# Kernel tuning notes

Measured on AMD Instinct MI355X. Metric: run time of the kernel, lower is better.

## Reference

```python
import jax, jax.numpy as jnp
from jax import lax
import numpy as np

POOLED_H = 7
POOLED_W = 7
SPATIAL_SCALE = 0.0625


def setup_inputs() -> dict:
    key = jax.random.key(0)
    kf, kx1, ky1, kw, kh = jax.random.split(key, 5)
    B, H, W, C = 1, 64, 64, 512
    N = 512
    img_h, img_w = H / SPATIAL_SCALE, W / SPATIAL_SCALE
    feat = jax.random.normal(kf, (B, H, W, C), dtype=jnp.float32)
    # rois: (batch_idx, x1, y1, x2, y2) in image coordinates, boxes inside image
    x1 = jax.random.uniform(kx1, (N,), minval=0.0, maxval=img_w * 0.8)
    y1 = jax.random.uniform(ky1, (N,), minval=0.0, maxval=img_h * 0.8)
    bw = jax.random.uniform(kw, (N,), minval=16.0, maxval=img_w * 0.5)
    bh = jax.random.uniform(kh, (N,), minval=16.0, maxval=img_h * 0.5)
    x2 = jnp.clip(x1 + bw, 0.0, img_w - 1.0)
    y2 = jnp.clip(y1 + bh, 0.0, img_h - 1.0)
    bidx = jnp.zeros((N,), dtype=jnp.float32)
    rois = jnp.stack([bidx, x1, y1, x2, y2], axis=1).astype(jnp.float32)
    return {"feat": feat, "rois": rois}


def _roi_pool(feat, rois, pooled_h, pooled_w, spatial_scale):
    B, H, W, C = feat.shape
    N = rois.shape[0]
    # max extent of a single bin (Caffe: hend-hstart <= bin_size + 2 <= H/pooled_h + 2)
    MBH = int(np.ceil(H / pooled_h)) + 2
    MBW = int(np.ceil(W / pooled_w)) + 2

    roi_batch = rois[:, 0].astype(jnp.int32)
    start_w = jnp.round(rois[:, 1] * spatial_scale).astype(jnp.int32)
    start_h = jnp.round(rois[:, 2] * spatial_scale).astype(jnp.int32)
    end_w = jnp.round(rois[:, 3] * spatial_scale).astype(jnp.int32)
    end_h = jnp.round(rois[:, 4] * spatial_scale).astype(jnp.int32)
    roi_h = jnp.maximum(end_h - start_h + 1, 1).astype(jnp.float32)
    roi_w = jnp.maximum(end_w - start_w + 1, 1).astype(jnp.float32)
    bin_h = roi_h / pooled_h  # [N] float
    bin_w = roi_w / pooled_w

    ar_h = jnp.arange(MBH)
    ar_w = jnp.arange(MBW)

    def pool_one_bin(bin_idx):
        ph = bin_idx // pooled_w
        pw = bin_idx % pooled_w

        def per_roi(b, sh, sw, bh_, bw_):
            hstart = jnp.clip(jnp.floor(ph * bh_).astype(jnp.int32) + sh, 0, H)
            hend = jnp.clip(jnp.ceil((ph + 1) * bh_).astype(jnp.int32) + sh, 0, H)
            wstart = jnp.clip(jnp.floor(pw * bw_).astype(jnp.int32) + sw, 0, W)
            wend = jnp.clip(jnp.ceil((pw + 1) * bw_).astype(jnp.int32) + sw, 0, W)
            empty = (hend <= hstart) | (wend <= wstart)
            # fixed-size window covering the bin; clamp start so slice stays in-bounds
            s_h = jnp.clip(hstart, 0, H - MBH)
            s_w = jnp.clip(wstart, 0, W - MBW)
            fmap = lax.dynamic_index_in_dim(feat, b, axis=0, keepdims=False)  # [H,W,C]
            patch = lax.dynamic_slice(fmap, (s_h, s_w, 0), (MBH, MBW, C))  # [MBH,MBW,C]
            rows = s_h + ar_h
            cols = s_w + ar_w
            valid = ((rows >= hstart) & (rows < hend))[:, None] & ((cols >= wstart) & (cols < wend))[None, :]
            neg = jnp.array(-jnp.inf, patch.dtype)
            mx = jnp.max(jnp.where(valid[:, :, None], patch, neg), axis=(0, 1))  # [C]
            return jnp.where(empty, jnp.zeros_like(mx), mx)

        return jax.vmap(per_roi)(roi_batch, start_h, start_w, bin_h, bin_w)  # [N,C]

    out = lax.map(pool_one_bin, jnp.arange(pooled_h * pooled_w))  # [PH*PW, N, C]
    out = out.transpose(1, 0, 2).reshape(N, pooled_h, pooled_w, C)
    return out


def reference(feat, rois):
    return _roi_pool(feat, rois, POOLED_H, POOLED_W, SPATIAL_SCALE)
```

## Files before the change

### kernel.cpp

```cpp
#include <hip/hip_runtime.h>
#include <cmath>

#define PH 7
#define PW 7
#define FH 64
#define FW 64
#define CC 512
#define SCALE 0.0625f

typedef float f32x4 __attribute__((ext_vector_type(4)));

static __device__ __forceinline__ f32x4 vmax4(f32x4 a, f32x4 b) {
    f32x4 r;
    r.x = fmaxf(a.x, b.x); r.y = fmaxf(a.y, b.y);
    r.z = fmaxf(a.z, b.z); r.w = fmaxf(a.w, b.w);
    return r;
}

__global__ __launch_bounds__(512) void sort_rois_kernel(
        const float* __restrict__ rois, int N, float4* __restrict__ geo) {
    __shared__ int base[64];
    __shared__ int cur[64];
    int t = threadIdx.x;
    if (t < 64) { base[t] = 0; cur[t] = 0; }
    __syncthreads();
    int b = -1, packed = 0;
    float bh = 0.f, bw = 0.f;
    if (t < N) {
        const float* r = rois + (size_t)t * 5;
        int bidx = (int)r[0];
        int sw = (int)rintf(r[1] * SCALE);
        int sh = (int)rintf(r[2] * SCALE);
        int ew = (int)rintf(r[3] * SCALE);
        int eh = (int)rintf(r[4] * SCALE);
        bh = fmaxf((float)(eh - sh + 1), 1.0f) * (1.0f / 7.0f);
        bw = fmaxf((float)(ew - sw + 1), 1.0f) * (1.0f / 7.0f);
        packed = t | (sh << 10) | (sw << 17) | (bidx << 24);
        b = min(max(sh, 0), FH - 1);
        atomicAdd(&base[b], 1);
    }
    __syncthreads();
    if (t == 0) {
        int acc = 0;
        for (int i = 0; i < 64; ++i) { int c = base[i]; base[i] = acc; acc += c; }
    }
    __syncthreads();
    if (t < N) {
        int pos = base[b] + atomicAdd(&cur[b], 1);
        float4 g;
        g.x = bh; g.y = bw; g.z = __int_as_float(packed); g.w = 0.f;
        geo[pos] = g;
    }
}

__global__ __launch_bounds__(256) void roi_pool_kernel(
        const float* __restrict__ feat,
        const float4* __restrict__ geo,
        float* __restrict__ out,
        int nBins) {
    int p = blockIdx.x;
    int nwg = gridDim.x;
    int q = nwg >> 3, rr = nwg & 7;
    int xcd = p & 7, o = p >> 3;
    int L = (xcd < rr ? xcd * (q + 1) : rr * (q + 1) + (xcd - rr) * q) + o;

    int tid = L * 256 + (int)threadIdx.x;
    int bin = tid >> 6;
    int lane = tid & 63;
    if (bin >= nBins) return;

    int s   = bin / (PH * PW);
    int rem = bin - s * (PH * PW);
    int ph  = rem / PW;
    int pw  = rem - ph * PW;

    float4 g = geo[s];
    float bh = g.x, bw = g.y;
    int packed = __float_as_int(g.z);
    int n    = packed & 1023;
    int sh   = (packed >> 10) & 127;
    int sw   = (packed >> 17) & 127;
    int bidx = (packed >> 24) & 255;

    int hstart = min(max((int)floorf((float)ph * bh) + sh, 0), FH);
    int hend   = min(max((int)ceilf((float)(ph + 1) * bh) + sh, 0), FH);
    int wstart = min(max((int)floorf((float)pw * bw) + sw, 0), FW);
    int wend   = min(max((int)ceilf((float)(pw + 1) * bw) + sw, 0), FW);

    int Wn = wend - wstart;
    int Hn = hend - hstart;
    bool empty = (Hn <= 0) || (Wn <= 0);

    f32x4 mxA = { -INFINITY, -INFINITY, -INFINITY, -INFINITY };
    f32x4 mxB = mxA;

    if (!empty) {
        unsigned cells = (unsigned)__builtin_amdgcn_readfirstlane(Hn * Wn);
        unsigned Wu    = (unsigned)__builtin_amdgcn_readfirstlane(Wn);
        unsigned wrap  = (unsigned)__builtin_amdgcn_readfirstlane((FW - Wn + 1) * CC);
        unsigned off0  = (unsigned)__builtin_amdgcn_readfirstlane(
            (bidx * FH * FW + hstart * FW + wstart) * CC);

        const float* fb = feat + off0;
        unsigned vo = (unsigned)lane * 4;

        unsigned soff = 0;
        unsigned cw = Wu;
        unsigned c = 0;
        unsigned quads = (cells + 3) >> 2;

#define ADV() do { if (--cw == 0) { soff += wrap; cw = Wu; } else soff += CC; } while (0)

        for (; quads; --quads) {
            unsigned o0 = soff;                          ADV();
            unsigned o1 = (c + 1 < cells) ? soff : 0u;   ADV();
            unsigned o2 = (c + 2 < cells) ? soff : 0u;   ADV();
            unsigned o3 = (c + 3 < cells) ? soff : 0u;   ADV();
            c += 4;
            const float* p0 = fb + o0;
            const float* p1 = fb + o1;
            const float* p2 = fb + o2;
            const float* p3 = fb + o3;
            f32x4 a0 = *(const f32x4*)(p0 + vo);  f32x4 b0 = *(const f32x4*)(p0 + vo + 256);
            f32x4 a1 = *(const f32x4*)(p1 + vo);  f32x4 b1 = *(const f32x4*)(p1 + vo + 256);
            f32x4 a2 = *(const f32x4*)(p2 + vo);  f32x4 b2 = *(const f32x4*)(p2 + vo + 256);
            f32x4 a3 = *(const f32x4*)(p3 + vo);  f32x4 b3 = *(const f32x4*)(p3 + vo + 256);
            a0 = vmax4(a0, a1); a2 = vmax4(a2, a3);
            b0 = vmax4(b0, b1); b2 = vmax4(b2, b3);
            mxA = vmax4(mxA, vmax4(a0, a2));
            mxB = vmax4(mxB, vmax4(b0, b2));
        }
#undef ADV
    } else {
        mxA = (f32x4){0.f, 0.f, 0.f, 0.f};
        mxB = mxA;
    }

    float* op = out + ((size_t)n * (PH * PW) + rem) * CC + (size_t)lane * 4;
    __builtin_nontemporal_store(mxA, (f32x4*)op);
    __builtin_nontemporal_store(mxB, (f32x4*)(op + 256));
}

extern "C" void kernel_launch(void* const* d_in, const int* in_sizes, int n_in,
                              void* d_out, int out_size, void* d_ws, size_t ws_size,
                              hipStream_t stream) {
    const float* feat = (const float*)d_in[0];
    const float* rois = (const float*)d_in[1];
    float* out = (float*)d_out;
    float4* geo = (float4*)d_ws;

    int N = in_sizes[1] / 5;
    sort_rois_kernel<<<1, 512, 0, stream>>>(rois, N, geo);

    int nBins = N * PH * PW;
    int totalThreads = nBins * 64;
    int block = 256;
    int grid = (totalThreads + block - 1) / block;
    roi_pool_kernel<<<grid, block, 0, stream>>>(feat, geo, out, nBins);
}
```

Baseline: 34.35 us.

## Process one pooled row per wavefront and reuse shared boundary column maxima

Each wavefront now handles a whole pooled row (7 bins) of one ROI instead of a single bin. It walks the columns once, computing a per-column max over the bin's rows. A column shared between adjacent bins (the ceil/floor overlap) is reused rather than reloaded. This cuts redundant feature loads at bin boundaries and per-bin index setup, but reduces the wave count 7x and serialises the bins within a wave, which lowers memory-level parallelism and occupancy.

```diff
diff --git a/kernel.cpp b/kernel.cpp
--- a/kernel.cpp
+++ b/kernel.cpp
@@ -57,22 +57,17 @@
         const float* __restrict__ feat,
         const float4* __restrict__ geo,
         float* __restrict__ out,
-        int nBins) {
-    int p = blockIdx.x;
-    int nwg = gridDim.x;
+        int nRows) {
+    int p = blockIdx.x, nwg = gridDim.x;
     int q = nwg >> 3, rr = nwg & 7;
     int xcd = p & 7, o = p >> 3;
     int L = (xcd < rr ? xcd * (q + 1) : rr * (q + 1) + (xcd - rr) * q) + o;
 
-    int tid = L * 256 + (int)threadIdx.x;
-    int bin = tid >> 6;
-    int lane = tid & 63;
-    if (bin >= nBins) return;
-
-    int s   = bin / (PH * PW);
-    int rem = bin - s * (PH * PW);
-    int ph  = rem / PW;
-    int pw  = rem - ph * PW;
+    int lane = (int)threadIdx.x & 63;
+    int wid = __builtin_amdgcn_readfirstlane(L * 4 + ((int)threadIdx.x >> 6));
+    if (wid >= nRows) return;
+    int s  = wid / 7;
+    int ph = wid - s * 7;
 
     float4 g = geo[s];
     float bh = g.x, bw = g.y;
@@ -82,63 +77,78 @@
     int sw   = (packed >> 17) & 127;
     int bidx = (packed >> 24) & 255;
 
-    int hstart = min(max((int)floorf((float)ph * bh) + sh, 0), FH);
-    int hend   = min(max((int)ceilf((float)(ph + 1) * bh) + sh, 0), FH);
-    int wstart = min(max((int)floorf((float)pw * bw) + sw, 0), FW);
-    int wend   = min(max((int)ceilf((float)(pw + 1) * bw) + sw, 0), FW);
+    int hs = min(max((int)floorf((float)ph * bh) + sh, 0), FH);
+    int he = min(max((int)ceilf((float)(ph + 1) * bh) + sh, 0), FH);
+    int R  = he - hs;
 
-    int Wn = wend - wstart;
-    int Hn = hend - hstart;
-    bool empty = (Hn <= 0) || (Wn <= 0);
+    float* outB = out + (size_t)(n * 49 + ph * 7) * CC + (size_t)lane * 4;
+    const f32x4 zero4 = {0.f, 0.f, 0.f, 0.f};
+    const f32x4 negi  = {-INFINITY, -INFINITY, -INFINITY, -INFINITY};
 
-    f32x4 mxA = { -INFINITY, -INFINITY, -INFINITY, -INFINITY };
-    f32x4 mxB = mxA;
-
-    if (!empty) {
-        unsigned cells = (unsigned)__builtin_amdgcn_readfirstlane(Hn * Wn);
-        unsigned Wu    = (unsigned)__builtin_amdgcn_readfirstlane(Wn);
-        unsigned wrap  = (unsigned)__builtin_amdgcn_readfirstlane((FW - Wn + 1) * CC);
-        unsigned off0  = (unsigned)__builtin_amdgcn_readfirstlane(
-            (bidx * FH * FW + hstart * FW + wstart) * CC);
-
-        const float* fb = feat + off0;
-        unsigned vo = (unsigned)lane * 4;
-
-        unsigned soff = 0;
-        unsigned cw = Wu;
-        unsigned c = 0;
-        unsigned quads = (cells + 3) >> 2;
-
-#define ADV() do { if (--cw == 0) { soff += wrap; cw = Wu; } else soff += CC; } while (0)
-
-        for (; quads; --quads) {
-            unsigned o0 = soff;                          ADV();
-            unsigned o1 = (c + 1 < cells) ? soff : 0u;   ADV();
-            unsigned o2 = (c + 2 < cells) ? soff : 0u;   ADV();
-            unsigned o3 = (c + 3 < cells) ? soff : 0u;   ADV();
-            c += 4;
-            const float* p0 = fb + o0;
-            const float* p1 = fb + o1;
-            const float* p2 = fb + o2;
-            const float* p3 = fb + o3;
-            f32x4 a0 = *(const f32x4*)(p0 + vo);  f32x4 b0 = *(const f32x4*)(p0 + vo + 256);
-            f32x4 a1 = *(const f32x4*)(p1 + vo);  f32x4 b1 = *(const f32x4*)(p1 + vo + 256);
-            f32x4 a2 = *(const f32x4*)(p2 + vo);  f32x4 b2 = *(const f32x4*)(p2 + vo + 256);
-            f32x4 a3 = *(const f32x4*)(p3 + vo);  f32x4 b3 = *(const f32x4*)(p3 + vo + 256);
-            a0 = vmax4(a0, a1); a2 = vmax4(a2, a3);
-            b0 = vmax4(b0, b1); b2 = vmax4(b2, b3);
-            mxA = vmax4(mxA, vmax4(a0, a2));
-            mxB = vmax4(mxB, vmax4(b0, b2));
+    if (R <= 0) {
+        for (int pw = 0; pw < 7; ++pw) {
+            __builtin_nontemporal_store(zero4, (f32x4*)(outB + pw * CC));
+            __builtin_nontemporal_store(zero4, (f32x4*)(outB + pw * CC + 256));
         }
-#undef ADV
-    } else {
-        mxA = (f32x4){0.f, 0.f, 0.f, 0.f};
-        mxB = mxA;
+        return;
     }
 
-    float* op = out + ((size_t)n * (PH * PW) + rem) * CC + (size_t)lane * 4;
-    __builtin_nontemporal_store(mxA, (f32x4*)op);
-    __builtin_nontemporal_store(mxB, (f32x4*)(op + 256));
+    const float* fb = feat + (size_t)((bidx * FH + hs) * FW) * CC + (size_t)lane * 4;
+    const int RS = FW * CC;
+
+    f32x4 vLastA = negi, vLastB = negi;
+    int wdone = 0;
+
+    for (int pw = 0; pw < 7; ++pw) {
+        int ws = min(max((int)floorf((float)pw * bw) + sw, 0), FW);
+        int we = min(max((int)ceilf((float)(pw + 1) * bw) + sw, 0), FW);
+        if (we <= ws) {
+            __builtin_nontemporal_store(zero4, (f32x4*)(outB + pw * CC));
+            __builtin_nontemporal_store(zero4, (f32x4*)(outB + pw * CC + 256));
+            continue;
+        }
+        f32x4 accA = (wdone > ws) ? vLastA : negi;
+        f32x4 accB = (wdone > ws) ? vLastB : negi;
+        int wbeg = max(ws, wdone);
+        for (int w = wbeg; w < we; ++w) {
+            const float* cb = fb + (size_t)w * CC;
+            f32x4 cA = negi, cB = negi;
+            int r = 0;
+            for (; r + 4 <= R; r += 4) {
+                const float* p0 = cb + (size_t)(r + 0) * RS;
+                const float* p1 = cb + (size_t)(r + 1) * RS;
+                const float* p2 = cb + (size_t)(r + 2) * RS;
+                const float* p3 = cb + (size_t)(r + 3) * RS;
+                f32x4 a0 = *(const f32x4*)p0; f32x4 b0 = *(const f32x4*)(p0 + 256);
+                f32x4 a1 = *(const f32x4*)p1; f32x4 b1 = *(const f32x4*)(p1 + 256);
+                f32x4 a2 = *(const f32x4*)p2; f32x4 b2 = *(const f32x4*)(p2 + 256);
+                f32x4 a3 = *(const f32x4*)p3; f32x4 b3 = *(const f32x4*)(p3 + 256);
+                cA = vmax4(cA, vmax4(vmax4(a0, a1), vmax4(a2, a3)));
+                cB = vmax4(cB, vmax4(vmax4(b0, b1), vmax4(b2, b3)));
+            }
+            if (R & 2) {
+                const float* p0 = cb + (size_t)(r + 0) * RS;
+                const float* p1 = cb + (size_t)(r + 1) * RS;
+                f32x4 a0 = *(const f32x4*)p0; f32x4 b0 = *(const f32x4*)(p0 + 256);
+                f32x4 a1 = *(const f32x4*)p1; f32x4 b1 = *(const f32x4*)(p1 + 256);
+                cA = vmax4(cA, vmax4(a0, a1));
+                cB = vmax4(cB, vmax4(b0, b1));
+                r += 2;
+            }
+            if (R & 1) {
+                const float* p0 = cb + (size_t)r * RS;
+                f32x4 a0 = *(const f32x4*)p0; f32x4 b0 = *(const f32x4*)(p0 + 256);
+                cA = vmax4(cA, a0);
+                cB = vmax4(cB, b0);
+            }
+            accA = vmax4(accA, cA);
+            accB = vmax4(accB, cB);
+            vLastA = cA; vLastB = cB;
+        }
+        wdone = we;
+        __builtin_nontemporal_store(accA, (f32x4*)(outB + pw * CC));
+        __builtin_nontemporal_store(accB, (f32x4*)(outB + pw * CC + 256));
+    }
 }
 
 extern "C" void kernel_launch(void* const* d_in, const int* in_sizes, int n_in,
@@ -152,9 +162,9 @@
     int N = in_sizes[1] / 5;
     sort_rois_kernel<<<1, 512, 0, stream>>>(rois, N, geo);
 
-    int nBins = N * PH * PW;
-    int totalThreads = nBins * 64;
+    int nRows = N * PH;
+    int totalThreads = nRows * 64;
     int block = 256;
     int grid = (totalThreads + block - 1) / block;
-    roi_pool_kernel<<<grid, block, 0, stream>>>(feat, geo, out, nBins);
+    roi_pool_kernel<<<grid, block, 0, stream>>>(feat, geo, out, nRows);
 }
```

Result: slower. 41.38 us (+20.5%).
